# Performance work log

Measured on AMD Instinct MI355X. Metric: run time of the kernel, lower is better.

## Reference

```python
import math
import jax, jax.numpy as jnp
import numpy as np

D_MODEL = 768
NUM_HEADS = 12
D_K = D_MODEL // NUM_HEADS
THETA = 10000.0
MAX_SEQ_LEN = 4096
BATCH = 1
SEQ_LEN = 4096


def setup_inputs() -> dict:
    key = jax.random.key(0)
    k0, k1, k2, k3, k4 = jax.random.split(key, 5)
    scale = 0.02
    return {
        "in_features": jax.random.normal(k0, (BATCH, SEQ_LEN, D_MODEL), jnp.float32),
        "token_positions": jnp.arange(SEQ_LEN, dtype=jnp.int32),
        "q_proj": jax.random.normal(k1, (D_MODEL, D_MODEL), jnp.float32) * scale,
        "k_proj": jax.random.normal(k2, (D_MODEL, D_MODEL), jnp.float32) * scale,
        "v_proj": jax.random.normal(k3, (D_MODEL, D_MODEL), jnp.float32) * scale,
        "o_proj": jax.random.normal(k4, (D_MODEL, D_MODEL), jnp.float32) * scale,
    }


def _apply_rope(x, token_positions):
    # x: (B, H, S, d_k) ; token_positions: (S,) int
    inv_freq = 1.0 / (THETA ** (jnp.arange(0, D_K, 2, dtype=jnp.float32) / D_K))  # (d_k//2,)
    pos = jnp.clip(token_positions, 0, MAX_SEQ_LEN - 1).astype(jnp.float32)
    freq = pos[:, None] * inv_freq[None, :]                 # (S, d_k//2)
    cos, sin = jnp.cos(freq), jnp.sin(freq)
    xr = x.reshape(*x.shape[:-1], D_K // 2, 2)              # interleaved pairs
    x0, x1 = xr[..., 0], xr[..., 1]                         # (B, H, S, d_k//2)
    x0r = x0 * cos - x1 * sin
    x1r = x0 * sin + x1 * cos
    return jnp.stack((x0r, x1r), axis=-1).reshape(x.shape)


def reference(in_features, token_positions, q_proj, k_proj, v_proj, o_proj):
    B, S, D = in_features.shape
    H, dk = NUM_HEADS, D_K

    def proj_heads(W):
        y = jnp.matmul(in_features, W.T)                    # (B, S, D)
        return y.reshape(B, S, H, dk).transpose(0, 2, 1, 3)  # (B, H, S, dk)

    Q = _apply_rope(proj_heads(q_proj), token_positions)
    K = _apply_rope(proj_heads(k_proj), token_positions)
    V = proj_heads(v_proj)

    score = jnp.einsum("bhqd,bhkd->bhqk", Q, K) / math.sqrt(dk)
    causal = jnp.triu(jnp.ones((S, S), dtype=bool), k=1)    # True above diagonal
    score = jnp.where(causal[None, None], -jnp.inf, score)
    attn = jax.nn.softmax(score, axis=-1)
    out = jnp.einsum("bhqk,bhkd->bhqd", attn, V)            # (B, H, S, dk)
    out = out.transpose(0, 2, 1, 3).reshape(B, S, D)
    return jnp.matmul(out, o_proj.T)
```

## Files before the change

kernel.cpp:

```cpp
#include <hip/hip_runtime.h>
#include <hip/hip_bf16.h>

#define S_LEN 4096
#define DM    768
#define NH    12
#define DKH   64

typedef __attribute__((ext_vector_type(8))) short short8;
typedef __attribute__((ext_vector_type(4))) float f32x4;

__device__ __forceinline__ short f2bf(float f) {
    union { float f; unsigned u; } v; v.f = f;
    unsigned r = (v.u + 0x7FFFu + ((v.u >> 16) & 1u)) >> 16;
    return (short)r;
}

#define MFMA16(a, b, c) __builtin_amdgcn_mfma_f32_16x16x32_bf16((a), (b), (c), 0, 0, 0)

__device__ __forceinline__ void cvt4(const float* __restrict__ s,
                                     short* __restrict__ d, int i) {
    float4 v = *reinterpret_cast<const float4*>(s + i);
    short4 o;
    o.x = f2bf(v.x); o.y = f2bf(v.y); o.z = f2bf(v.z); o.w = f2bf(v.w);
    *reinterpret_cast<short4*>(d + i) = o;
}

__global__ __launch_bounds__(256) void prep_k(
    const float* __restrict__ X, const float* __restrict__ Wq,
    const float* __restrict__ Wk, const float* __restrict__ Wv,
    const float* __restrict__ Wo, const int* __restrict__ pos,
    short* __restrict__ Xbf, short* __restrict__ Wqb, short* __restrict__ Wkb,
    short* __restrict__ Wvb, short* __restrict__ Wob, float2* __restrict__ rt) {
    const int bx = blockIdx.x, tid = threadIdx.x;
    if (bx < 3072)      cvt4(X,  Xbf, bx * 1024 + tid * 4);
    else if (bx < 3648) cvt4(Wq, Wqb, (bx - 3072) * 1024 + tid * 4);
    else if (bx < 4224) cvt4(Wk, Wkb, (bx - 3648) * 1024 + tid * 4);
    else if (bx < 4800) cvt4(Wv, Wvb, (bx - 4224) * 1024 + tid * 4);
    else if (bx < 5376) cvt4(Wo, Wob, (bx - 4800) * 1024 + tid * 4);
    else {
        int idx = (bx - 5376) * 256 + tid;
        int s = idx >> 5, i = idx & 31;
        int p = pos[s]; p = p < 0 ? 0 : (p > 4095 ? 4095 : p);
        double inv = pow(10000.0, -(double)i / 32.0);
        float ang = (float)((double)p * inv);
        rt[idx] = make_float2(cosf(ang), sinf(ang));
    }
}

__device__ __forceinline__ void gemm_mainloop(const short* __restrict__ A,
                                              const short* __restrict__ B,
                                              short* Al, short* Bl,
                                              int m0, int n0, int t,
                                              f32x4 acc[4][4]) {
    const int wave = t >> 6, lane = t & 63;
    const int wm = (wave >> 1) * 64, wn = (wave & 1) * 64;
    const int l15 = lane & 15, lg = lane >> 4;
    const int grow = lane >> 3;
    const int gch = (lane & 7) ^ grow;
    const int dsto = wave * 512 + lane * 8;

#define GEMM_STAGE(k0, buf)                                                          \
    {                                                                                \
        _Pragma("unroll")                                                            \
        for (int i = 0; i < 4; ++i) {                                                \
            int row = i * 32 + wave * 8 + grow;                                      \
            __builtin_amdgcn_global_load_lds(                                        \
                (const __attribute__((address_space(1))) void*)                      \
                    &A[(m0 + row) * DM + (k0) + gch * 8],                            \
                (__attribute__((address_space(3))) void*)                            \
                    (Al + (buf) * 8192 + i * 2048 + dsto), 16, 0, 0);                \
            __builtin_amdgcn_global_load_lds(                                        \
                (const __attribute__((address_space(1))) void*)                      \
                    &B[(n0 + row) * DM + (k0) + gch * 8],                            \
                (__attribute__((address_space(3))) void*)                            \
                    (Bl + (buf) * 8192 + i * 2048 + dsto), 16, 0, 0);                \
        }                                                                            \
    }

    GEMM_STAGE(0, 0);
    asm volatile("s_waitcnt vmcnt(0)" ::: "memory");
    __builtin_amdgcn_s_barrier();

    const int NSTEP = DM / 64;
    for (int step = 0; step < NSTEP; ++step) {
        const int cur = step & 1;
        if (step + 1 < NSTEP) GEMM_STAGE((step + 1) * 64, cur ^ 1);
        __builtin_amdgcn_sched_barrier(0);
        const short* Ab_ = Al + cur * 8192;
        const short* Bb_ = Bl + cur * 8192;
#pragma unroll
        for (int kh = 0; kh < 2; ++kh) {
            const int c8 = (kh * 4 + lg) ^ (l15 & 7);
            short8 af[4], bf[4];
#pragma unroll
            for (int m = 0; m < 4; ++m)
                af[m] = *reinterpret_cast<const short8*>(Ab_ + (wm + m * 16 + l15) * 64 + c8 * 8);
#pragma unroll
            for (int n = 0; n < 4; ++n)
                bf[n] = *reinterpret_cast<const short8*>(Bb_ + (wn + n * 16 + l15) * 64 + c8 * 8);
#pragma unroll
            for (int m = 0; m < 4; ++m)
#pragma unroll
                for (int n = 0; n < 4; ++n)
                    acc[m][n] = MFMA16(af[m], bf[n], acc[m][n]);
        }
        asm volatile("s_waitcnt vmcnt(0)" ::: "memory");
        __builtin_amdgcn_sched_barrier(0);
        __builtin_amdgcn_s_barrier();
    }
#undef GEMM_STAGE
}

__global__ __launch_bounds__(256) void gemm_qkv_k(
    const short* __restrict__ Xbf, const short* __restrict__ Wq,
    const short* __restrict__ Wk, const short* __restrict__ Wv,
    const float2* __restrict__ rt,
    short* __restrict__ Q, short* __restrict__ K, short* __restrict__ Vt) {
    __shared__ __align__(16) short Al[2 * 128 * 64];
    __shared__ __align__(16) short Bl[2 * 128 * 64];
    const int mat = blockIdx.z;
    const short* B = mat == 0 ? Wq : (mat == 1 ? Wk : Wv);
    const int m0 = blockIdx.y * 128, n0 = blockIdx.x * 128;
    const int t = threadIdx.x;
    f32x4 acc[4][4] = {};
    gemm_mainloop(Xbf, B, Al, Bl, m0, n0, t, acc);
    const int wave = t >> 6, lane = t & 63;
    const int wm = (wave >> 1) * 64, wn = (wave & 1) * 64;
    const int l15 = lane & 15, lg = lane >> 4;
    if (mat < 2) {
        short* Out = mat == 0 ? Q : K;
        const float qs = 0.125f * 1.44269504088896f;
#pragma unroll
        for (int m = 0; m < 4; ++m) {
#pragma unroll
            for (int n = 0; n < 4; ++n) {
                int col = n0 + wn + n * 16 + l15;
                int h = col >> 6, d = col & 63;
#pragma unroll
                for (int j = 0; j < 4; ++j) {
                    int srow = m0 + wm + m * 16 + lg * 4 + j;
                    float v = acc[m][n][j];
                    float other = __shfl_xor(v, 1);
                    float2 cs = rt[srow * 32 + (d >> 1)];
                    v = (d & 1) ? (other * cs.y + v * cs.x)
                                : (v * cs.x - other * cs.y);
                    if (mat == 0) v *= qs;
                    Out[(h * S_LEN + srow) * DKH + d] = f2bf(v);
                }
            }
        }
    } else {
#pragma unroll
        for (int m = 0; m < 4; ++m)
#pragma unroll
            for (int n = 0; n < 4; ++n) {
                int col = n0 + wn + n * 16 + l15;
                int h = col >> 6, d = col & 63;
                int srow0 = m0 + wm + m * 16 + lg * 4;
                short4 b;
                b.x = f2bf(acc[m][n][0]); b.y = f2bf(acc[m][n][1]);
                b.z = f2bf(acc[m][n][2]); b.w = f2bf(acc[m][n][3]);
                *reinterpret_cast<short4*>(&Vt[(size_t)(h * DKH + d) * S_LEN + srow0]) = b;
            }
    }
}

__global__ __launch_bounds__(256) void gemm_out_k(const short* __restrict__ Ab,
                                                  const short* __restrict__ Wo,
                                                  float* __restrict__ out) {
    __shared__ __align__(16) short Al[2 * 128 * 64];
    __shared__ __align__(16) short Bl[2 * 128 * 64];
    const int m0 = blockIdx.y * 128, n0 = blockIdx.x * 128;
    const int t = threadIdx.x;
    f32x4 acc[4][4] = {};
    gemm_mainloop(Ab, Wo, Al, Bl, m0, n0, t, acc);
    const int wave = t >> 6, lane = t & 63;
    const int wm = (wave >> 1) * 64, wn = (wave & 1) * 64;
    const int l15 = lane & 15, lg = lane >> 4;
#pragma unroll
    for (int m = 0; m < 4; ++m)
#pragma unroll
        for (int n = 0; n < 4; ++n)
#pragma unroll
            for (int j = 0; j < 4; ++j) {
                int srow = m0 + wm + m * 16 + lg * 4 + j;
                int col = n0 + wn + n * 16 + l15;
                out[srow * DM + col] = acc[m][n][j];
            }
}

__device__ __forceinline__ void stage64(const short* __restrict__ gRow0,
                                        int rowStride, short* lbuf,
                                        int wave, int lane) {
#pragma unroll
    for (int i = 0; i < 2; ++i) {
        int c = wave + i * 4;
        int row = c * 8 + (lane >> 3);
        int gch = (lane & 7) ^ (lane >> 3);
        const short* src = gRow0 + (long)row * rowStride + gch * 8;
        short* dst = lbuf + c * 512 + lane * 8;
        __builtin_amdgcn_global_load_lds(
            (const __attribute__((address_space(1))) void*)src,
            (__attribute__((address_space(3))) void*)dst, 16, 0, 0);
    }
}

__global__ __launch_bounds__(256) void attn_k(const short* __restrict__ Q,
                                              const short* __restrict__ K,
                                              const short* __restrict__ Vt,
                                              short* __restrict__ Aout) {
    const int bx = blockIdx.x;
    const int h = bx % NH;
    const int qb = (S_LEN / 64 - 1) - (bx / NH);
    const int t = threadIdx.x;
    const int wave = t >> 6, lane = t & 63;
    const int l15 = lane & 15, lg = lane >> 4;
    const int q0w = qb * 64 + wave * 16;

    __shared__ __align__(16) short KVl[2][2][64 * 64];
    __shared__ __align__(16) short Pl[4][16][76];

    const short* Kh = K + (size_t)h * S_LEN * DKH;
    const short* Vh = Vt + (size_t)h * DKH * S_LEN;

    short8 qf[2];
#pragma unroll
    for (int ks = 0; ks < 2; ++ks)
        qf[ks] = *reinterpret_cast<const short8*>(
            &Q[(h * S_LEN + q0w + l15) * DKH + ks * 32 + lg * 8]);

    f32x4 o[4] = {};
    float mrun = -1e30f, lpart = 0.f;
    const int nt = qb + 1;

    stage64(Kh, DKH, KVl[0][0], wave, lane);
    stage64(Vh, S_LEN, KVl[0][1], wave, lane);
    __syncthreads();

    for (int tile = 0; tile < nt; ++tile) {
        const int cur = tile & 1;
        if (tile + 1 < nt) {
            stage64(Kh + (size_t)(tile + 1) * 64 * DKH, DKH, KVl[cur ^ 1][0], wave, lane);
            stage64(Vh + (tile + 1) * 64, S_LEN, KVl[cur ^ 1][1], wave, lane);
        }
        __builtin_amdgcn_sched_barrier(0);
        const char* Kb = (const char*)KVl[cur][0];
        const char* Vb = (const char*)KVl[cur][1];

        f32x4 s[4] = {};
        __builtin_amdgcn_s_setprio(1);
#pragma unroll
        for (int ks = 0; ks < 2; ++ks)
#pragma unroll
            for (int n = 0; n < 4; ++n) {
                int r = n * 16 + l15;
                int c8 = (ks * 4 + lg) ^ (r & 7);
                short8 kf = *reinterpret_cast<const short8*>(Kb + r * 128 + c8 * 16);
                s[n] = MFMA16(kf, qf[ks], s[n]);
            }
        __builtin_amdgcn_s_setprio(0);

        if (tile == qb) {
            const int q = q0w + l15;
#pragma unroll
            for (int n = 0; n < 4; ++n)
#pragma unroll
                for (int j = 0; j < 4; ++j)
                    if (tile * 64 + n * 16 + lg * 4 + j > q) s[n][j] = -1e30f;
        }

        float mt = fmaxf(fmaxf(fmaxf(s[0][0], s[0][1]), fmaxf(s[0][2], s[0][3])),
                         fmaxf(fmaxf(s[1][0], s[1][1]), fmaxf(s[1][2], s[1][3])));
        mt = fmaxf(mt, fmaxf(fmaxf(fmaxf(s[2][0], s[2][1]), fmaxf(s[2][2], s[2][3])),
                             fmaxf(fmaxf(s[3][0], s[3][1]), fmaxf(s[3][2], s[3][3]))));

        if (__all(mt <= mrun + 8.f)) {
#pragma unroll
            for (int n = 0; n < 4; ++n)
#pragma unroll
                for (int j = 0; j < 4; ++j) {
                    float p = exp2f(s[n][j] - mrun);
                    s[n][j] = p;
                    lpart += p;
                }
        } else {
            float mm = fmaxf(mt, __shfl_xor(mt, 16));
            mm = fmaxf(mm, __shfl_xor(mm, 32));
            float mnew = fmaxf(mrun, mm);
            float alpha = exp2f(mrun - mnew);
            lpart *= alpha;
#pragma unroll
            for (int n = 0; n < 4; ++n)
#pragma unroll
                for (int j = 0; j < 4; ++j) {
                    float p = exp2f(s[n][j] - mnew);
                    s[n][j] = p;
                    lpart += p;
                }
#pragma unroll
            for (int n = 0; n < 4; ++n)
#pragma unroll
                for (int j = 0; j < 4; ++j) o[n][j] *= alpha;
            mrun = mnew;
        }

#pragma unroll
        for (int n = 0; n < 4; ++n) {
            unsigned p0, p1;
            asm("v_cvt_pk_bf16_f32 %0, %1, %2" : "=v"(p0) : "v"(s[n][0]), "v"(s[n][1]));
            asm("v_cvt_pk_bf16_f32 %0, %1, %2" : "=v"(p1) : "v"(s[n][2]), "v"(s[n][3]));
            uint2 w; w.x = p0; w.y = p1;
            *reinterpret_cast<uint2*>(&Pl[wave][l15][n * 16 + lg * 4]) = w;
        }

        __builtin_amdgcn_s_setprio(1);
#pragma unroll
        for (int ks = 0; ks < 2; ++ks) {
            short8 pa = *reinterpret_cast<const short8*>(
                &Pl[wave][l15][ks * 32 + lg * 8]);
#pragma unroll
            for (int n = 0; n < 4; ++n) {
                int r = n * 16 + l15;
                int c8 = (ks * 4 + lg) ^ (r & 7);
                short8 vf = *reinterpret_cast<const short8*>(Vb + r * 128 + c8 * 16);
                o[n] = MFMA16(vf, pa, o[n]);
            }
        }
        __builtin_amdgcn_s_setprio(0);

        asm volatile("s_waitcnt vmcnt(0)" ::: "memory");
        __builtin_amdgcn_sched_barrier(0);
        __builtin_amdgcn_s_barrier();
    }

    float lsum = lpart + __shfl_xor(lpart, 16);
    lsum += __shfl_xor(lsum, 32);
    float inv = 1.f / lsum;

    __syncthreads();
    float* Ol = (float*)&KVl[0][0][0] + wave * (16 * 68);
#pragma unroll
    for (int n = 0; n < 4; ++n) {
        float4 w;
        w.x = o[n][0] * inv; w.y = o[n][1] * inv;
        w.z = o[n][2] * inv; w.w = o[n][3] * inv;
        *reinterpret_cast<float4*>(&Ol[l15 * 68 + n * 16 + lg * 4]) = w;
    }
#pragma unroll
    for (int kk = 0; kk < 4; ++kk) {
        int r = lane >> 2, c0 = (lane & 3) * 4 + kk * 16;
        float4 v = *reinterpret_cast<const float4*>(&Ol[r * 68 + c0]);
        short4 b;
        b.x = f2bf(v.x); b.y = f2bf(v.y); b.z = f2bf(v.z); b.w = f2bf(v.w);
        *reinterpret_cast<short4*>(
            &Aout[(size_t)(q0w + r) * DM + h * DKH + c0]) = b;
    }
}

extern "C" void kernel_launch(void* const* d_in, const int* in_sizes, int n_in,
                              void* d_out, int out_size, void* d_ws, size_t ws_size,
                              hipStream_t stream) {
    const float* X  = (const float*)d_in[0];
    const int*   pos = (const int*)d_in[1];
    const float* Wq = (const float*)d_in[2];
    const float* Wk = (const float*)d_in[3];
    const float* Wv = (const float*)d_in[4];
    const float* Wo = (const float*)d_in[5];
    float* out = (float*)d_out;

    char* ws = (char*)d_ws;
    short* Xbf = (short*)ws;  ws += (size_t)S_LEN * DM * 2;
    short* Wqb = (short*)ws;  ws += (size_t)DM * DM * 2;
    short* Wkb = (short*)ws;  ws += (size_t)DM * DM * 2;
    short* Wvb = (short*)ws;  ws += (size_t)DM * DM * 2;
    short* Wob = (short*)ws;  ws += (size_t)DM * DM * 2;
    float2* rt = (float2*)ws; ws += (size_t)S_LEN * 32 * 8;
    short* Qb  = (short*)ws;  ws += (size_t)NH * S_LEN * DKH * 2;
    short* Kb  = (short*)ws;  ws += (size_t)NH * S_LEN * DKH * 2;
    short* Vtb = (short*)ws;  ws += (size_t)NH * S_LEN * DKH * 2;
    short* Ab  = (short*)ws;  ws += (size_t)S_LEN * DM * 2;

    prep_k<<<5888, 256, 0, stream>>>(X, Wq, Wk, Wv, Wo, pos,
                                     Xbf, Wqb, Wkb, Wvb, Wob, rt);
    gemm_qkv_k<<<dim3(6, 32, 3), 256, 0, stream>>>(Xbf, Wqb, Wkb, Wvb, rt, Qb, Kb, Vtb);
    attn_k<<<dim3(64 * NH), 256, 0, stream>>>(Qb, Kb, Vtb, Ab);
    gemm_out_k<<<dim3(6, 32), 256, 0, stream>>>(Ab, Wob, out);
}
```

Baseline: 147.7 us.

## Split attention KV range across waves with per-wave softmax state and merge

Reworks the attention kernel so all four waves share the same 64 query rows but each wave walks a disjoint, interleaved subset of 32-wide KV tiles with its own private double-buffered LDS staging. The per-wave partial max, sum and output accumulators are merged through LDS at the end, flash-decoding style. This drops the per-tile block barrier and reuses each K/V fragment across four query fragments, with the aim of cutting LDS traffic and synchronisation stalls. In exchange it uses 64KB of LDS, more registers for the 4x4 accumulators, and adds a cross-wave reduction epilogue.

```diff
diff --git a/kernel.cpp b/kernel.cpp
--- a/kernel.cpp
+++ b/kernel.cpp
@@ -5,6 +5,9 @@
 #define DM    768
 #define NH    12
 #define DKH   64
+
+#define AS1 __attribute__((address_space(1)))
+#define AS3 __attribute__((address_space(3)))
 
 typedef __attribute__((ext_vector_type(8))) short short8;
 typedef __attribute__((ext_vector_type(4))) float f32x4;
@@ -65,15 +68,11 @@
         for (int i = 0; i < 4; ++i) {                                                \
             int row = i * 32 + wave * 8 + grow;                                      \
             __builtin_amdgcn_global_load_lds(                                        \
-                (const __attribute__((address_space(1))) void*)                      \
-                    &A[(m0 + row) * DM + (k0) + gch * 8],                            \
-                (__attribute__((address_space(3))) void*)                            \
-                    (Al + (buf) * 8192 + i * 2048 + dsto), 16, 0, 0);                \
+                (const AS1 void*)&A[(m0 + row) * DM + (k0) + gch * 8],               \
+                (AS3 void*)(Al + (buf) * 8192 + i * 2048 + dsto), 16, 0, 0);         \
             __builtin_amdgcn_global_load_lds(                                        \
-                (const __attribute__((address_space(1))) void*)                      \
-                    &B[(n0 + row) * DM + (k0) + gch * 8],                            \
-                (__attribute__((address_space(3))) void*)                            \
-                    (Bl + (buf) * 8192 + i * 2048 + dsto), 16, 0, 0);                \
+                (const AS1 void*)&B[(n0 + row) * DM + (k0) + gch * 8],               \
+                (AS3 void*)(Bl + (buf) * 8192 + i * 2048 + dsto), 16, 0, 0);         \
         }                                                                            \
     }
 
@@ -189,171 +188,249 @@
             }
 }
 
-__device__ __forceinline__ void stage64(const short* __restrict__ gRow0,
-                                        int rowStride, short* lbuf,
-                                        int wave, int lane) {
-#pragma unroll
-    for (int i = 0; i < 2; ++i) {
-        int c = wave + i * 4;
-        int row = c * 8 + (lane >> 3);
-        int gch = (lane & 7) ^ (lane >> 3);
-        const short* src = gRow0 + (long)row * rowStride + gch * 8;
-        short* dst = lbuf + c * 512 + lane * 8;
+
+__device__ __forceinline__ void stageK32(const short* __restrict__ Kh, int kv0,
+                                         short* dst, int lane) {
+#pragma unroll
+    for (int i = 0; i < 4; ++i) {
+        int id = i * 64 + lane;
+        int row = id >> 3, ch = id & 7;
+        int gch = ch ^ (row & 7);
         __builtin_amdgcn_global_load_lds(
-            (const __attribute__((address_space(1))) void*)src,
-            (__attribute__((address_space(3))) void*)dst, 16, 0, 0);
-    }
-}
-
-__global__ __launch_bounds__(256) void attn_k(const short* __restrict__ Q,
-                                              const short* __restrict__ K,
-                                              const short* __restrict__ Vt,
-                                              short* __restrict__ Aout) {
+            (const AS1 void*)&Kh[(kv0 + row) * DKH + gch * 8],
+            (AS3 void*)(dst + id * 8), 16, 0, 0);
+    }
+}
+
+__device__ __forceinline__ void stageV32(const short* __restrict__ Vh, int kv0,
+                                         short* dst, int lane) {
+#pragma unroll
+    for (int i = 0; i < 4; ++i) {
+        int id = i * 64 + lane;
+        int row = id >> 2, ch = id & 3;
+        int gch = ch ^ ((row >> 1) & 3);
+        __builtin_amdgcn_global_load_lds(
+            (const AS1 void*)&Vh[row * S_LEN + kv0 + gch * 8],
+            (AS3 void*)(dst + id * 8), 16, 0, 0);
+    }
+}
+
+__global__ __launch_bounds__(256, 2) void attn_k(const short* __restrict__ Q,
+                                                 const short* __restrict__ K,
+                                                 const short* __restrict__ Vt,
+                                                 short* __restrict__ Aout) {
     const int bx = blockIdx.x;
     const int h = bx % NH;
     const int qb = (S_LEN / 64 - 1) - (bx / NH);
+    const int q0 = qb * 64;
     const int t = threadIdx.x;
     const int wave = t >> 6, lane = t & 63;
     const int l15 = lane & 15, lg = lane >> 4;
-    const int q0w = qb * 64 + wave * 16;
-
-    __shared__ __align__(16) short KVl[2][2][64 * 64];
-    __shared__ __align__(16) short Pl[4][16][76];
+    const int swz = (l15 >> 1) & 3;
+
+    __shared__ __align__(16) char SMEM[65536];
+    short* WB = (short*)(SMEM + wave * 16384);
 
     const short* Kh = K + (size_t)h * S_LEN * DKH;
     const short* Vh = Vt + (size_t)h * DKH * S_LEN;
 
-    short8 qf[2];
-#pragma unroll
-    for (int ks = 0; ks < 2; ++ks)
-        qf[ks] = *reinterpret_cast<const short8*>(
-            &Q[(h * S_LEN + q0w + l15) * DKH + ks * 32 + lg * 8]);
-
-    f32x4 o[4] = {};
-    float mrun = -1e30f, lpart = 0.f;
-    const int nt = qb + 1;
-
-    stage64(Kh, DKH, KVl[0][0], wave, lane);
-    stage64(Vh, S_LEN, KVl[0][1], wave, lane);
+    short8 qf[4][2];
+#pragma unroll
+    for (int f = 0; f < 4; ++f)
+#pragma unroll
+        for (int ks = 0; ks < 2; ++ks)
+            qf[f][ks] = *reinterpret_cast<const short8*>(
+                &Q[(h * S_LEN + q0 + f * 16 + l15) * DKH + ks * 32 + lg * 8]);
+
+    f32x4 o[4][4] = {};
+    float mrun[4], lpart[4];
+#pragma unroll
+    for (int f = 0; f < 4; ++f) { mrun[f] = -1e30f; lpart[f] = 0.f; }
+
+    const int nt = 2 * qb + 2;
+    if (wave < nt) {
+        stageK32(Kh, wave * 32, WB, lane);
+        stageV32(Vh, wave * 32, WB + 4096, lane);
+    }
+    int cur = 0;
+
+    for (int mt = wave; mt < nt; mt += 4) {
+        const bool pre = (mt + 4 < nt);
+        if (pre) {
+            stageK32(Kh, (mt + 4) * 32, WB + (cur ^ 1) * 2048, lane);
+            stageV32(Vh, (mt + 4) * 32, WB + 4096 + (cur ^ 1) * 2048, lane);
+        }
+        __builtin_amdgcn_sched_barrier(0);
+        if (pre) asm volatile("s_waitcnt vmcnt(8)" ::: "memory");
+        else     asm volatile("s_waitcnt vmcnt(0)" ::: "memory");
+        __builtin_amdgcn_sched_barrier(0);
+        short* Kb = WB + cur * 2048;
+        short* Vb = WB + 4096 + cur * 2048;
+
+        f32x4 s[2][4] = {};
+        __builtin_amdgcn_s_setprio(1);
+#pragma unroll
+        for (int ks = 0; ks < 2; ++ks)
+#pragma unroll
+            for (int n = 0; n < 2; ++n) {
+                short8 kf = *reinterpret_cast<const short8*>(
+                    Kb + (n * 16 + l15) * 64 + (((ks * 4 + lg) ^ (l15 & 7)) * 8));
+#pragma unroll
+                for (int f = 0; f < 4; ++f)
+                    s[n][f] = MFMA16(kf, qf[f][ks], s[n][f]);
+            }
+        __builtin_amdgcn_s_setprio(0);
+
+        if (mt >= 2 * qb) {
+#pragma unroll
+            for (int n = 0; n < 2; ++n)
+#pragma unroll
+                for (int f = 0; f < 4; ++f) {
+                    const int q = q0 + f * 16 + l15;
+#pragma unroll
+                    for (int j = 0; j < 4; ++j)
+                        if (mt * 32 + n * 16 + lg * 4 + j > q) s[n][f][j] = -1e30f;
+                }
+        }
+
+        float mx[4];
+#pragma unroll
+        for (int f = 0; f < 4; ++f)
+            mx[f] = fmaxf(fmaxf(fmaxf(s[0][f][0], s[0][f][1]), fmaxf(s[0][f][2], s[0][f][3])),
+                          fmaxf(fmaxf(s[1][f][0], s[1][f][1]), fmaxf(s[1][f][2], s[1][f][3])));
+
+        bool loc = (mx[0] <= mrun[0] + 8.f) && (mx[1] <= mrun[1] + 8.f) &&
+                   (mx[2] <= mrun[2] + 8.f) && (mx[3] <= mrun[3] + 8.f);
+        if (__all(loc)) {
+#pragma unroll
+            for (int n = 0; n < 2; ++n)
+#pragma unroll
+                for (int f = 0; f < 4; ++f)
+#pragma unroll
+                    for (int j = 0; j < 4; ++j) {
+                        float p = exp2f(s[n][f][j] - mrun[f]);
+                        s[n][f][j] = p;
+                        lpart[f] += p;
+                    }
+        } else {
+#pragma unroll
+            for (int f = 0; f < 4; ++f) {
+                float mm = fmaxf(mx[f], __shfl_xor(mx[f], 16));
+                mm = fmaxf(mm, __shfl_xor(mm, 32));
+                float mnew = fmaxf(mrun[f], mm);
+                float alpha = exp2f(mrun[f] - mnew);
+                lpart[f] *= alpha;
+#pragma unroll
+                for (int n = 0; n < 2; ++n)
+#pragma unroll
+                    for (int j = 0; j < 4; ++j) {
+                        float p = exp2f(s[n][f][j] - mnew);
+                        s[n][f][j] = p;
+                        lpart[f] += p;
+                    }
+#pragma unroll
+                for (int n = 0; n < 4; ++n) o[n][f] *= alpha;
+                mrun[f] = mnew;
+            }
+        }
+
+#pragma unroll
+        for (int f = 0; f < 4; ++f)
+#pragma unroll
+            for (int n = 0; n < 2; ++n) {
+                unsigned p0, p1;
+                asm("v_cvt_pk_bf16_f32 %0, %1, %2" : "=v"(p0) : "v"(s[n][f][0]), "v"(s[n][f][1]));
+                asm("v_cvt_pk_bf16_f32 %0, %1, %2" : "=v"(p1) : "v"(s[n][f][2]), "v"(s[n][f][3]));
+                uint2 w; w.x = p0; w.y = p1;
+                int chp = (n * 2 + (lg >> 1)) ^ swz;
+                *reinterpret_cast<uint2*>(
+                    Kb + (f * 16 + l15) * 32 + chp * 8 + (lg & 1) * 4) = w;
+            }
+
+        __builtin_amdgcn_s_setprio(1);
+        short8 pa[4];
+#pragma unroll
+        for (int f = 0; f < 4; ++f)
+            pa[f] = *reinterpret_cast<const short8*>(
+                Kb + (f * 16 + l15) * 32 + ((lg ^ swz)) * 8);
+#pragma unroll
+        for (int n = 0; n < 4; ++n) {
+            short8 vf = *reinterpret_cast<const short8*>(
+                Vb + (n * 16 + l15) * 32 + ((lg ^ swz)) * 8);
+#pragma unroll
+            for (int f = 0; f < 4; ++f)
+                o[n][f] = MFMA16(vf, pa[f], o[n][f]);
+        }
+        __builtin_amdgcn_s_setprio(0);
+        cur ^= 1;
+    }
+
+    float scl[4][4], ltot[4];
+    {
+        float lsum[4];
+#pragma unroll
+        for (int f = 0; f < 4; ++f) {
+            float ls = lpart[f] + __shfl_xor(lpart[f], 16);
+            ls += __shfl_xor(ls, 32);
+            lsum[f] = ls;
+        }
+        float2* ML = (float2*)WB;
+        if (lane < 16) {
+#pragma unroll
+            for (int f = 0; f < 4; ++f)
+                ML[f * 16 + l15] = make_float2(mrun[f], lsum[f]);
+        }
+        __syncthreads();
+#pragma unroll
+        for (int f = 0; f < 4; ++f) {
+            float mv[4], lv[4], m = -1e30f;
+#pragma unroll
+            for (int w = 0; w < 4; ++w) {
+                float2 x = *((const float2*)(SMEM + w * 16384) + f * 16 + l15);
+                mv[w] = x.x; lv[w] = x.y;
+                m = fmaxf(m, x.x);
+            }
+            float lt = 0.f;
+#pragma unroll
+            for (int w = 0; w < 4; ++w) {
+                float sc = exp2f(mv[w] - m);
+                scl[w][f] = sc;
+                lt += sc * lv[w];
+            }
+            ltot[f] = lt;
+        }
+        __syncthreads();
+    }
+#pragma unroll
+    for (int n = 0; n < 4; ++n)
+#pragma unroll
+        for (int f = 0; f < 4; ++f)
+            *reinterpret_cast<f32x4*>((char*)WB + ((n * 4 + f) * 64 + lane) * 16) = o[n][f];
     __syncthreads();
-
-    for (int tile = 0; tile < nt; ++tile) {
-        const int cur = tile & 1;
-        if (tile + 1 < nt) {
-            stage64(Kh + (size_t)(tile + 1) * 64 * DKH, DKH, KVl[cur ^ 1][0], wave, lane);
-            stage64(Vh + (tile + 1) * 64, S_LEN, KVl[cur ^ 1][1], wave, lane);
-        }
-        __builtin_amdgcn_sched_barrier(0);
-        const char* Kb = (const char*)KVl[cur][0];
-        const char* Vb = (const char*)KVl[cur][1];
-
-        f32x4 s[4] = {};
-        __builtin_amdgcn_s_setprio(1);
-#pragma unroll
-        for (int ks = 0; ks < 2; ++ks)
-#pragma unroll
-            for (int n = 0; n < 4; ++n) {
-                int r = n * 16 + l15;
-                int c8 = (ks * 4 + lg) ^ (r & 7);
-                short8 kf = *reinterpret_cast<const short8*>(Kb + r * 128 + c8 * 16);
-                s[n] = MFMA16(kf, qf[ks], s[n]);
-            }
-        __builtin_amdgcn_s_setprio(0);
-
-        if (tile == qb) {
-            const int q = q0w + l15;
-#pragma unroll
-            for (int n = 0; n < 4; ++n)
-#pragma unroll
-                for (int j = 0; j < 4; ++j)
-                    if (tile * 64 + n * 16 + lg * 4 + j > q) s[n][j] = -1e30f;
-        }
-
-        float mt = fmaxf(fmaxf(fmaxf(s[0][0], s[0][1]), fmaxf(s[0][2], s[0][3])),
-                         fmaxf(fmaxf(s[1][0], s[1][1]), fmaxf(s[1][2], s[1][3])));
-        mt = fmaxf(mt, fmaxf(fmaxf(fmaxf(s[2][0], s[2][1]), fmaxf(s[2][2], s[2][3])),
-                             fmaxf(fmaxf(s[3][0], s[3][1]), fmaxf(s[3][2], s[3][3]))));
-
-        if (__all(mt <= mrun + 8.f)) {
-#pragma unroll
-            for (int n = 0; n < 4; ++n)
-#pragma unroll
-                for (int j = 0; j < 4; ++j) {
-                    float p = exp2f(s[n][j] - mrun);
-                    s[n][j] = p;
-                    lpart += p;
-                }
-        } else {
-            float mm = fmaxf(mt, __shfl_xor(mt, 16));
-            mm = fmaxf(mm, __shfl_xor(mm, 32));
-            float mnew = fmaxf(mrun, mm);
-            float alpha = exp2f(mrun - mnew);
-            lpart *= alpha;
-#pragma unroll
-            for (int n = 0; n < 4; ++n)
-#pragma unroll
-                for (int j = 0; j < 4; ++j) {
-                    float p = exp2f(s[n][j] - mnew);
-                    s[n][j] = p;
-                    lpart += p;
-                }
-#pragma unroll
-            for (int n = 0; n < 4; ++n)
-#pragma unroll
-                for (int j = 0; j < 4; ++j) o[n][j] *= alpha;
-            mrun = mnew;
-        }
-
-#pragma unroll
-        for (int n = 0; n < 4; ++n) {
-            unsigned p0, p1;
-            asm("v_cvt_pk_bf16_f32 %0, %1, %2" : "=v"(p0) : "v"(s[n][0]), "v"(s[n][1]));
-            asm("v_cvt_pk_bf16_f32 %0, %1, %2" : "=v"(p1) : "v"(s[n][2]), "v"(s[n][3]));
-            uint2 w; w.x = p0; w.y = p1;
-            *reinterpret_cast<uint2*>(&Pl[wave][l15][n * 16 + lg * 4]) = w;
-        }
-
-        __builtin_amdgcn_s_setprio(1);
-#pragma unroll
-        for (int ks = 0; ks < 2; ++ks) {
-            short8 pa = *reinterpret_cast<const short8*>(
-                &Pl[wave][l15][ks * 32 + lg * 8]);
-#pragma unroll
-            for (int n = 0; n < 4; ++n) {
-                int r = n * 16 + l15;
-                int c8 = (ks * 4 + lg) ^ (r & 7);
-                short8 vf = *reinterpret_cast<const short8*>(Vb + r * 128 + c8 * 16);
-                o[n] = MFMA16(vf, pa, o[n]);
-            }
-        }
-        __builtin_amdgcn_s_setprio(0);
-
-        asm volatile("s_waitcnt vmcnt(0)" ::: "memory");
-        __builtin_amdgcn_sched_barrier(0);
-        __builtin_amdgcn_s_barrier();
-    }
-
-    float lsum = lpart + __shfl_xor(lpart, 16);
-    lsum += __shfl_xor(lsum, 32);
-    float inv = 1.f / lsum;
-
+    f32x4 otot[4] = {};
+#pragma unroll
+    for (int w = 0; w < 4; ++w)
+#pragma unroll
+        for (int f = 0; f < 4; ++f) {
+            f32x4 po = *reinterpret_cast<const f32x4*>(
+                SMEM + w * 16384 + ((wave * 4 + f) * 64 + lane) * 16);
+            otot[f] += po * scl[w][f];
+        }
     __syncthreads();
-    float* Ol = (float*)&KVl[0][0][0] + wave * (16 * 68);
-#pragma unroll
-    for (int n = 0; n < 4; ++n) {
-        float4 w;
-        w.x = o[n][0] * inv; w.y = o[n][1] * inv;
-        w.z = o[n][2] * inv; w.w = o[n][3] * inv;
-        *reinterpret_cast<float4*>(&Ol[l15 * 68 + n * 16 + lg * 4]) = w;
-    }
-#pragma unroll
-    for (int kk = 0; kk < 4; ++kk) {
-        int r = lane >> 2, c0 = (lane & 3) * 4 + kk * 16;
-        float4 v = *reinterpret_cast<const float4*>(&Ol[r * 68 + c0]);
+    float* T = (float*)WB;
+#pragma unroll
+    for (int f = 0; f < 4; ++f) {
+        f32x4 w = otot[f] * (1.f / ltot[f]);
+        *reinterpret_cast<f32x4*>(T + (f * 16 + l15) * 20 + lg * 4) = w;
+    }
+#pragma unroll
+    for (int it = 0; it < 4; ++it) {
+        int q = it * 16 + (lane >> 2), d4 = (lane & 3) * 4;
+        f32x4 v = *reinterpret_cast<const f32x4*>(T + q * 20 + d4);
         short4 b;
-        b.x = f2bf(v.x); b.y = f2bf(v.y); b.z = f2bf(v.z); b.w = f2bf(v.w);
+        b.x = f2bf(v[0]); b.y = f2bf(v[1]); b.z = f2bf(v[2]); b.w = f2bf(v[3]);
         *reinterpret_cast<short4*>(
-            &Aout[(size_t)(q0w + r) * DM + h * DKH + c0]) = b;
+            &Aout[(size_t)(q0 + q) * DM + h * DKH + wave * 16 + d4]) = b;
     }
 }
 
```

Result: slower. 199.9 us (+35.4%).

## Split long causal attention rows into two KV segments with combine kernel

Applied to the files above, without the earlier changes.

Query blocks 32..63, which hold the longest causal KV ranges, are each split into two KV segments handled by separate workgroups. The attention grid grows from 768 to 1152 blocks. The split blocks write unnormalized partial outputs plus (max, sum) statistics to fp32 workspace, and a new combine kernel merges the two segments and writes bf16 output. This aims to balance the causal triangular workload and fill more CUs, at the cost of an extra launch and extra fp32 traffic for the partials.

```diff
diff --git a/kernel.cpp b/kernel.cpp
--- a/kernel.cpp
+++ b/kernel.cpp
@@ -5,6 +5,9 @@
 #define DM    768
 #define NH    12
 #define DKH   64
+
+#define AS1 __attribute__((address_space(1)))
+#define AS3 __attribute__((address_space(3)))
 
 typedef __attribute__((ext_vector_type(8))) short short8;
 typedef __attribute__((ext_vector_type(4))) float f32x4;
@@ -65,15 +68,11 @@
         for (int i = 0; i < 4; ++i) {                                                \
             int row = i * 32 + wave * 8 + grow;                                      \
             __builtin_amdgcn_global_load_lds(                                        \
-                (const __attribute__((address_space(1))) void*)                      \
-                    &A[(m0 + row) * DM + (k0) + gch * 8],                            \
-                (__attribute__((address_space(3))) void*)                            \
-                    (Al + (buf) * 8192 + i * 2048 + dsto), 16, 0, 0);                \
+                (const AS1 void*)&A[(m0 + row) * DM + (k0) + gch * 8],               \
+                (AS3 void*)(Al + (buf) * 8192 + i * 2048 + dsto), 16, 0, 0);         \
             __builtin_amdgcn_global_load_lds(                                        \
-                (const __attribute__((address_space(1))) void*)                      \
-                    &B[(n0 + row) * DM + (k0) + gch * 8],                            \
-                (__attribute__((address_space(3))) void*)                            \
-                    (Bl + (buf) * 8192 + i * 2048 + dsto), 16, 0, 0);                \
+                (const AS1 void*)&B[(n0 + row) * DM + (k0) + gch * 8],               \
+                (AS3 void*)(Bl + (buf) * 8192 + i * 2048 + dsto), 16, 0, 0);         \
         }                                                                            \
     }
 
@@ -200,18 +199,25 @@
         const short* src = gRow0 + (long)row * rowStride + gch * 8;
         short* dst = lbuf + c * 512 + lane * 8;
         __builtin_amdgcn_global_load_lds(
-            (const __attribute__((address_space(1))) void*)src,
-            (__attribute__((address_space(3))) void*)dst, 16, 0, 0);
+            (const AS1 void*)src, (AS3 void*)dst, 16, 0, 0);
     }
 }
 
 __global__ __launch_bounds__(256) void attn_k(const short* __restrict__ Q,
                                               const short* __restrict__ K,
                                               const short* __restrict__ Vt,
-                                              short* __restrict__ Aout) {
+                                              short* __restrict__ Aout,
+                                              float* __restrict__ Op,
+                                              float2* __restrict__ Mp) {
     const int bx = blockIdx.x;
     const int h = bx % NH;
-    const int qb = (S_LEN / 64 - 1) - (bx / NH);
+    const int sid = bx / NH;
+    const int qb = (sid < 32) ? (63 - sid) : (95 - sid);
+    const bool partial = (sid < 64);
+    const int seg = (sid >= 32 && sid < 64) ? 1 : 0;
+    const int t0 = seg ? 32 : 0;
+    const int t1 = (sid < 32) ? 32 : (qb + 1);
+
     const int t = threadIdx.x;
     const int wave = t >> 6, lane = t & 63;
     const int l15 = lane & 15, lg = lane >> 4;
@@ -231,15 +237,14 @@
 
     f32x4 o[4] = {};
     float mrun = -1e30f, lpart = 0.f;
-    const int nt = qb + 1;
-
-    stage64(Kh, DKH, KVl[0][0], wave, lane);
-    stage64(Vh, S_LEN, KVl[0][1], wave, lane);
+
+    stage64(Kh + (size_t)t0 * 64 * DKH, DKH, KVl[0][0], wave, lane);
+    stage64(Vh + t0 * 64, S_LEN, KVl[0][1], wave, lane);
     __syncthreads();
 
-    for (int tile = 0; tile < nt; ++tile) {
-        const int cur = tile & 1;
-        if (tile + 1 < nt) {
+    for (int tile = t0; tile < t1; ++tile) {
+        const int cur = (tile - t0) & 1;
+        if (tile + 1 < t1) {
             stage64(Kh + (size_t)(tile + 1) * 64 * DKH, DKH, KVl[cur ^ 1][0], wave, lane);
             stage64(Vh + (tile + 1) * 64, S_LEN, KVl[cur ^ 1][1], wave, lane);
         }
@@ -335,25 +340,75 @@
 
     float lsum = lpart + __shfl_xor(lpart, 16);
     lsum += __shfl_xor(lsum, 32);
-    float inv = 1.f / lsum;
 
     __syncthreads();
     float* Ol = (float*)&KVl[0][0][0] + wave * (16 * 68);
-#pragma unroll
-    for (int n = 0; n < 4; ++n) {
-        float4 w;
-        w.x = o[n][0] * inv; w.y = o[n][1] * inv;
-        w.z = o[n][2] * inv; w.w = o[n][3] * inv;
-        *reinterpret_cast<float4*>(&Ol[l15 * 68 + n * 16 + lg * 4]) = w;
-    }
-#pragma unroll
-    for (int kk = 0; kk < 4; ++kk) {
-        int r = lane >> 2, c0 = (lane & 3) * 4 + kk * 16;
-        float4 v = *reinterpret_cast<const float4*>(&Ol[r * 68 + c0]);
-        short4 b;
-        b.x = f2bf(v.x); b.y = f2bf(v.y); b.z = f2bf(v.z); b.w = f2bf(v.w);
-        *reinterpret_cast<short4*>(
-            &Aout[(size_t)(q0w + r) * DM + h * DKH + c0]) = b;
+
+    if (partial) {
+#pragma unroll
+        for (int n = 0; n < 4; ++n) {
+            float4 w;
+            w.x = o[n][0]; w.y = o[n][1]; w.z = o[n][2]; w.w = o[n][3];
+            *reinterpret_cast<float4*>(&Ol[l15 * 68 + n * 16 + lg * 4]) = w;
+        }
+        const size_t rowbase = ((size_t)h * 32 + (qb - 32)) * 64;
+        const size_t segR = (size_t)NH * 32 * 64;
+        if (lane < 16)
+            Mp[seg * segR + rowbase + wave * 16 + l15] = make_float2(mrun, lsum);
+#pragma unroll
+        for (int kk = 0; kk < 4; ++kk) {
+            int r = lane >> 2, c0 = (lane & 3) * 4 + kk * 16;
+            float4 v = *reinterpret_cast<const float4*>(&Ol[r * 68 + c0]);
+            *reinterpret_cast<float4*>(
+                &Op[(seg * segR + rowbase + wave * 16 + r) * 64 + c0]) = v;
+        }
+    } else {
+        float inv = 1.f / lsum;
+#pragma unroll
+        for (int n = 0; n < 4; ++n) {
+            float4 w;
+            w.x = o[n][0] * inv; w.y = o[n][1] * inv;
+            w.z = o[n][2] * inv; w.w = o[n][3] * inv;
+            *reinterpret_cast<float4*>(&Ol[l15 * 68 + n * 16 + lg * 4]) = w;
+        }
+#pragma unroll
+        for (int kk = 0; kk < 4; ++kk) {
+            int r = lane >> 2, c0 = (lane & 3) * 4 + kk * 16;
+            float4 v = *reinterpret_cast<const float4*>(&Ol[r * 68 + c0]);
+            short4 b;
+            b.x = f2bf(v.x); b.y = f2bf(v.y); b.z = f2bf(v.z); b.w = f2bf(v.w);
+            *reinterpret_cast<short4*>(
+                &Aout[(size_t)(q0w + r) * DM + h * DKH + c0]) = b;
+        }
+    }
+}
+
+__global__ __launch_bounds__(256) void combine_k(const float* __restrict__ Op,
+                                                 const float2* __restrict__ Mp,
+                                                 short* __restrict__ Aout) {
+    const int h = blockIdx.x / 32, qbr = blockIdx.x % 32;
+    const int t = threadIdx.x;
+    const int row = t >> 2, c0 = (t & 3) * 16;
+    const size_t rowbase = ((size_t)h * 32 + qbr) * 64 + row;
+    const size_t segR = (size_t)NH * 32 * 64;
+    float2 ml0 = Mp[rowbase], ml1 = Mp[segR + rowbase];
+    float m = fmaxf(ml0.x, ml1.x);
+    float s0 = exp2f(ml0.x - m), s1 = exp2f(ml1.x - m);
+    float inv = 1.f / (s0 * ml0.y + s1 * ml1.y);
+    const float* O0 = Op + rowbase * 64;
+    const float* O1 = Op + (segR + rowbase) * 64;
+    const int q = (32 + qbr) * 64 + row;
+#pragma unroll
+    for (int i = 0; i < 4; ++i) {
+        int d = c0 + i * 4;
+        float4 a = *reinterpret_cast<const float4*>(O0 + d);
+        float4 b = *reinterpret_cast<const float4*>(O1 + d);
+        short4 r;
+        r.x = f2bf((a.x * s0 + b.x * s1) * inv);
+        r.y = f2bf((a.y * s0 + b.y * s1) * inv);
+        r.z = f2bf((a.z * s0 + b.z * s1) * inv);
+        r.w = f2bf((a.w * s0 + b.w * s1) * inv);
+        *reinterpret_cast<short4*>(&Aout[(size_t)q * DM + h * DKH + d]) = r;
     }
 }
 
@@ -379,10 +434,13 @@
     short* Kb  = (short*)ws;  ws += (size_t)NH * S_LEN * DKH * 2;
     short* Vtb = (short*)ws;  ws += (size_t)NH * S_LEN * DKH * 2;
     short* Ab  = (short*)ws;  ws += (size_t)S_LEN * DM * 2;
+    float* Op  = (float*)ws;  ws += (size_t)2 * NH * 32 * 64 * 64 * 4;
+    float2* Mp = (float2*)ws; ws += (size_t)2 * NH * 32 * 64 * 8;
 
     prep_k<<<5888, 256, 0, stream>>>(X, Wq, Wk, Wv, Wo, pos,
                                      Xbf, Wqb, Wkb, Wvb, Wob, rt);
     gemm_qkv_k<<<dim3(6, 32, 3), 256, 0, stream>>>(Xbf, Wqb, Wkb, Wvb, rt, Qb, Kb, Vtb);
-    attn_k<<<dim3(64 * NH), 256, 0, stream>>>(Qb, Kb, Vtb, Ab);
+    attn_k<<<dim3(96 * NH), 256, 0, stream>>>(Qb, Kb, Vtb, Ab, Op, Mp);
+    combine_k<<<dim3(NH * 32), 256, 0, stream>>>(Op, Mp, Ab);
     gemm_out_k<<<dim3(6, 32), 256, 0, stream>>>(Ab, Wob, out);
 }
```

Result: faster. 135.5 us (-8.2%).
